# Kernel tuning notes

Hardware: AMD Instinct MI355X
Metric: run time of the kernel (lower is better)

The kernel has to match this reference:

```python
import jax, jax.numpy as jnp
import numpy as np

DIM = 2048
NUM_EXPERTS = 4
EPS = 1e-6
SCALE = 3.0


def setup_inputs() -> dict:
    key = jax.random.key(0)
    k_x, k_w = jax.random.split(key)
    x = jax.random.normal(k_x, (4, 8192, DIM), dtype=jnp.float32)
    norm_weight = jnp.ones((DIM,), dtype=jnp.float32)
    router_weight = jax.random.normal(k_w, (NUM_EXPERTS, DIM), dtype=jnp.float32) * (1.0 / np.sqrt(DIM))
    return {"x": x, "norm_weight": norm_weight, "router_weight": router_weight}


def reference(x, norm_weight, router_weight):
    # RMSNorm over last dim
    rms = jnp.sqrt(jnp.mean(x * x, axis=-1, keepdims=True) + EPS)
    xn = x / rms * norm_weight
    # tiny router projection: [b, s, d] @ [e, d]^T -> [b, s, e]
    logits = jnp.einsum('bsd,ed->bse', xn, router_weight) * SCALE
    return jnp.tanh(logits)
```

## Files before the change

### kernel.cpp

```cpp
#include <hip/hip_runtime.h>
#include <cmath>

constexpr int   DIM   = 2048;
constexpr int   NEXP  = 4;
constexpr float EPS   = 1e-6f;
constexpr float SCALE = 3.0f;

__global__ __launch_bounds__(256, 2)
void altup_router_kernel(const float* __restrict__ x,
                         const float* __restrict__ nw,
                         const float* __restrict__ rw,
                         float* __restrict__ out,
                         int nrows)
{
    const int lane          = threadIdx.x & 63;
    const int wid_in_blk    = threadIdx.x >> 6;
    const int waves_per_blk = blockDim.x >> 6;
    const int nwaves        = gridDim.x * waves_per_blk;
    const int wave          = blockIdx.x * waves_per_blk + wid_in_blk;

    const int base = lane * 4;

    float4 w[NEXP][8];
#pragma unroll
    for (int e = 0; e < NEXP; ++e) {
#pragma unroll
        for (int k = 0; k < 8; ++k) {
            const int d = k * 256 + base;
            const float4 r = *reinterpret_cast<const float4*>(rw + e * DIM + d);
            const float4 n = *reinterpret_cast<const float4*>(nw + d);
            w[e][k] = make_float4(r.x * n.x, r.y * n.y, r.z * n.z, r.w * n.w);
        }
    }

    for (int row = wave; row < nrows; row += nwaves) {
        const float* xr = x + (size_t)row * DIM;

        float acc[5] = {0.f, 0.f, 0.f, 0.f, 0.f};
#pragma unroll
        for (int k = 0; k < 8; ++k) {
            const float4 xv = *reinterpret_cast<const float4*>(xr + k * 256 + base);

            acc[0] = fmaf(xv.x, xv.x, acc[0]);
            acc[0] = fmaf(xv.y, xv.y, acc[0]);
            acc[0] = fmaf(xv.z, xv.z, acc[0]);
            acc[0] = fmaf(xv.w, xv.w, acc[0]);
#pragma unroll
            for (int e = 0; e < NEXP; ++e) {
                acc[1 + e] = fmaf(xv.x, w[e][k].x, acc[1 + e]);
                acc[1 + e] = fmaf(xv.y, w[e][k].y, acc[1 + e]);
                acc[1 + e] = fmaf(xv.z, w[e][k].z, acc[1 + e]);
                acc[1 + e] = fmaf(xv.w, w[e][k].w, acc[1 + e]);
            }
        }

#pragma unroll
        for (int m = 32; m >= 1; m >>= 1) {
#pragma unroll
            for (int i = 0; i < 5; ++i)
                acc[i] += __shfl_xor(acc[i], m, 64);
        }

        if (lane == 0) {
            const float inv_rms = rsqrtf(acc[0] * (1.0f / DIM) + EPS);
            float4 o;
            o.x = tanhf(acc[1] * inv_rms * SCALE);
            o.y = tanhf(acc[2] * inv_rms * SCALE);
            o.z = tanhf(acc[3] * inv_rms * SCALE);
            o.w = tanhf(acc[4] * inv_rms * SCALE);
            reinterpret_cast<float4*>(out)[row] = o;
        }
    }
}

extern "C" void kernel_launch(void* const* d_in, const int* in_sizes, int n_in,
                              void* d_out, int out_size, void* d_ws, size_t ws_size,
                              hipStream_t stream)
{
    const float* x   = (const float*)d_in[0];
    const float* nw  = (const float*)d_in[1];
    const float* rw  = (const float*)d_in[2];
    float*       out = (float*)d_out;

    const int nrows = in_sizes[0] / DIM;

    int waves_needed  = (nrows + 7) / 8;
    int blocks        = (waves_needed + 3) / 4;
    if (blocks > 1024) blocks = 1024;
    if (blocks < 1)    blocks = 1;

    hipLaunchKernelGGL(altup_router_kernel, dim3(blocks), dim3(256), 0, stream,
                       x, nw, rw, out, nrows);
}
```

Measured before the change: 49.30 us.

## Stage router weights in LDS and process two rows per wave

```diff
diff --git a/kernel.cpp b/kernel.cpp
--- a/kernel.cpp
+++ b/kernel.cpp
@@ -6,69 +6,97 @@
 constexpr float EPS   = 1e-6f;
 constexpr float SCALE = 3.0f;
 
-__global__ __launch_bounds__(256, 2)
+__global__ __launch_bounds__(256, 4)
 void altup_router_kernel(const float* __restrict__ x,
                          const float* __restrict__ nw,
                          const float* __restrict__ rw,
                          float* __restrict__ out,
                          int nrows)
 {
-    const int lane          = threadIdx.x & 63;
-    const int wid_in_blk    = threadIdx.x >> 6;
-    const int waves_per_blk = blockDim.x >> 6;
-    const int nwaves        = gridDim.x * waves_per_blk;
-    const int wave          = blockIdx.x * waves_per_blk + wid_in_blk;
+    __shared__ float wlds[NEXP * DIM];
 
-    const int base = lane * 4;
+    const int tid = threadIdx.x;
 
-    float4 w[NEXP][8];
-#pragma unroll
-    for (int e = 0; e < NEXP; ++e) {
+    for (int i = tid * 4; i < NEXP * DIM; i += 256 * 4) {
+        const int d = i & (DIM - 1);
+        const float4 r = *reinterpret_cast<const float4*>(rw + i);
+        const float4 n = *reinterpret_cast<const float4*>(nw + d);
+        *reinterpret_cast<float4*>(wlds + i) =
+            make_float4(r.x * n.x, r.y * n.y, r.z * n.z, r.w * n.w);
+    }
+    __syncthreads();
+
+    const int lane   = tid & 63;
+    const int wid    = tid >> 6;
+    const int nwaves = gridDim.x * (blockDim.x >> 6);
+    const int wave   = blockIdx.x * (blockDim.x >> 6) + wid;
+    const int base   = lane * 4;
+
+    const int npairs = (nrows + 1) >> 1;
+
+    for (int pr = wave; pr < npairs; pr += nwaves) {
+        const int row  = pr * 2;
+        const bool two = (row + 1) < nrows;
+
+        const float* xr0 = x + (size_t)row * DIM;
+        const float* xr1 = xr0 + (two ? DIM : 0);
+
+        float acc[10] = {0.f};
+
 #pragma unroll
         for (int k = 0; k < 8; ++k) {
             const int d = k * 256 + base;
-            const float4 r = *reinterpret_cast<const float4*>(rw + e * DIM + d);
-            const float4 n = *reinterpret_cast<const float4*>(nw + d);
-            w[e][k] = make_float4(r.x * n.x, r.y * n.y, r.z * n.z, r.w * n.w);
-        }
-    }
+            const float4 a = *reinterpret_cast<const float4*>(xr0 + d);
+            const float4 b = *reinterpret_cast<const float4*>(xr1 + d);
 
-    for (int row = wave; row < nrows; row += nwaves) {
-        const float* xr = x + (size_t)row * DIM;
+            acc[0] = fmaf(a.x, a.x, acc[0]);
+            acc[0] = fmaf(a.y, a.y, acc[0]);
+            acc[0] = fmaf(a.z, a.z, acc[0]);
+            acc[0] = fmaf(a.w, a.w, acc[0]);
+            acc[5] = fmaf(b.x, b.x, acc[5]);
+            acc[5] = fmaf(b.y, b.y, acc[5]);
+            acc[5] = fmaf(b.z, b.z, acc[5]);
+            acc[5] = fmaf(b.w, b.w, acc[5]);
 
-        float acc[5] = {0.f, 0.f, 0.f, 0.f, 0.f};
-#pragma unroll
-        for (int k = 0; k < 8; ++k) {
-            const float4 xv = *reinterpret_cast<const float4*>(xr + k * 256 + base);
-
-            acc[0] = fmaf(xv.x, xv.x, acc[0]);
-            acc[0] = fmaf(xv.y, xv.y, acc[0]);
-            acc[0] = fmaf(xv.z, xv.z, acc[0]);
-            acc[0] = fmaf(xv.w, xv.w, acc[0]);
 #pragma unroll
             for (int e = 0; e < NEXP; ++e) {
-                acc[1 + e] = fmaf(xv.x, w[e][k].x, acc[1 + e]);
-                acc[1 + e] = fmaf(xv.y, w[e][k].y, acc[1 + e]);
-                acc[1 + e] = fmaf(xv.z, w[e][k].z, acc[1 + e]);
-                acc[1 + e] = fmaf(xv.w, w[e][k].w, acc[1 + e]);
+                const float4 w = *reinterpret_cast<const float4*>(wlds + e * DIM + d);
+                acc[1 + e] = fmaf(a.x, w.x, acc[1 + e]);
+                acc[1 + e] = fmaf(a.y, w.y, acc[1 + e]);
+                acc[1 + e] = fmaf(a.z, w.z, acc[1 + e]);
+                acc[1 + e] = fmaf(a.w, w.w, acc[1 + e]);
+                acc[6 + e] = fmaf(b.x, w.x, acc[6 + e]);
+                acc[6 + e] = fmaf(b.y, w.y, acc[6 + e]);
+                acc[6 + e] = fmaf(b.z, w.z, acc[6 + e]);
+                acc[6 + e] = fmaf(b.w, w.w, acc[6 + e]);
             }
         }
 
 #pragma unroll
         for (int m = 32; m >= 1; m >>= 1) {
 #pragma unroll
-            for (int i = 0; i < 5; ++i)
+            for (int i = 0; i < 10; ++i)
                 acc[i] += __shfl_xor(acc[i], m, 64);
         }
 
         if (lane == 0) {
-            const float inv_rms = rsqrtf(acc[0] * (1.0f / DIM) + EPS);
-            float4 o;
-            o.x = tanhf(acc[1] * inv_rms * SCALE);
-            o.y = tanhf(acc[2] * inv_rms * SCALE);
-            o.z = tanhf(acc[3] * inv_rms * SCALE);
-            o.w = tanhf(acc[4] * inv_rms * SCALE);
-            reinterpret_cast<float4*>(out)[row] = o;
+            const float ir0 = rsqrtf(acc[0] * (1.0f / DIM) + EPS);
+            float4 o0;
+            o0.x = tanhf(acc[1] * ir0 * SCALE);
+            o0.y = tanhf(acc[2] * ir0 * SCALE);
+            o0.z = tanhf(acc[3] * ir0 * SCALE);
+            o0.w = tanhf(acc[4] * ir0 * SCALE);
+            reinterpret_cast<float4*>(out)[row] = o0;
+
+            if (two) {
+                const float ir1 = rsqrtf(acc[5] * (1.0f / DIM) + EPS);
+                float4 o1;
+                o1.x = tanhf(acc[6] * ir1 * SCALE);
+                o1.y = tanhf(acc[7] * ir1 * SCALE);
+                o1.z = tanhf(acc[8] * ir1 * SCALE);
+                o1.w = tanhf(acc[9] * ir1 * SCALE);
+                reinterpret_cast<float4*>(out)[row + 1] = o1;
+            }
         }
     }
 }
@@ -82,12 +110,13 @@
     const float* rw  = (const float*)d_in[2];
     float*       out = (float*)d_out;
 
-    const int nrows = in_sizes[0] / DIM;
+    const int nrows  = in_sizes[0] / DIM;
+    const int npairs = (nrows + 1) >> 1;
 
-    int waves_needed  = (nrows + 7) / 8;
-    int blocks        = (waves_needed + 3) / 4;
-    if (blocks > 1024) blocks = 1024;
-    if (blocks < 1)    blocks = 1;
+    int blocks = 512;
+    const int max_blocks = (npairs + 3) / 4;
+    if (blocks > max_blocks) blocks = max_blocks;
+    if (blocks < 1) blocks = 1;
 
     hipLaunchKernelGGL(altup_router_kernel, dim3(blocks), dim3(256), 0, stream,
                        x, nw, rw, out, nrows);
```

Result: slower. 117.1 us (+137.5%).

## Double-buffer row loads with contiguous per-wave chunks and nontemporal loads

Applied to the files above, without the earlier changes.

```diff
diff --git a/kernel.cpp b/kernel.cpp
--- a/kernel.cpp
+++ b/kernel.cpp
@@ -6,70 +6,91 @@
 constexpr float EPS   = 1e-6f;
 constexpr float SCALE = 3.0f;
 
+typedef float f32x4 __attribute__((ext_vector_type(4)));
+
 __global__ __launch_bounds__(256, 2)
 void altup_router_kernel(const float* __restrict__ x,
                          const float* __restrict__ nw,
                          const float* __restrict__ rw,
                          float* __restrict__ out,
-                         int nrows)
+                         int nrows, int chunk)
 {
-    const int lane          = threadIdx.x & 63;
-    const int wid_in_blk    = threadIdx.x >> 6;
-    const int waves_per_blk = blockDim.x >> 6;
-    const int nwaves        = gridDim.x * waves_per_blk;
-    const int wave          = blockIdx.x * waves_per_blk + wid_in_blk;
-
+    const int tid  = threadIdx.x;
+    const int lane = tid & 63;
+    const int wid  = tid >> 6;
+    const int wave = blockIdx.x * (blockDim.x >> 6) + wid;
     const int base = lane * 4;
 
-    float4 w[NEXP][8];
+    f32x4 w[NEXP][8];
 #pragma unroll
     for (int e = 0; e < NEXP; ++e) {
 #pragma unroll
         for (int k = 0; k < 8; ++k) {
             const int d = k * 256 + base;
-            const float4 r = *reinterpret_cast<const float4*>(rw + e * DIM + d);
-            const float4 n = *reinterpret_cast<const float4*>(nw + d);
-            w[e][k] = make_float4(r.x * n.x, r.y * n.y, r.z * n.z, r.w * n.w);
+            const f32x4 r = *reinterpret_cast<const f32x4*>(rw + e * DIM + d);
+            const f32x4 n = *reinterpret_cast<const f32x4*>(nw + d);
+            w[e][k] = r * n;
         }
     }
 
-    for (int row = wave; row < nrows; row += nwaves) {
+    int r    = wave * chunk;
+    int rend = r + chunk;
+    if (rend > nrows) rend = nrows;
+    if (r >= rend) return;
+
+    f32x4 bufA[8], bufB[8];
+
+    auto LOAD = [&](f32x4 (&buf)[8], int row) {
         const float* xr = x + (size_t)row * DIM;
+#pragma unroll
+        for (int k = 0; k < 8; ++k)
+            buf[k] = __builtin_nontemporal_load(
+                         reinterpret_cast<const f32x4*>(xr + k * 256 + base));
+    };
 
+    auto PROC = [&](const f32x4 (&buf)[8], int row) {
         float acc[5] = {0.f, 0.f, 0.f, 0.f, 0.f};
 #pragma unroll
         for (int k = 0; k < 8; ++k) {
-            const float4 xv = *reinterpret_cast<const float4*>(xr + k * 256 + base);
-
-            acc[0] = fmaf(xv.x, xv.x, acc[0]);
-            acc[0] = fmaf(xv.y, xv.y, acc[0]);
-            acc[0] = fmaf(xv.z, xv.z, acc[0]);
-            acc[0] = fmaf(xv.w, xv.w, acc[0]);
+            const f32x4 a = buf[k];
+#pragma unroll
+            for (int j = 0; j < 4; ++j)
+                acc[0] = fmaf(a[j], a[j], acc[0]);
 #pragma unroll
             for (int e = 0; e < NEXP; ++e) {
-                acc[1 + e] = fmaf(xv.x, w[e][k].x, acc[1 + e]);
-                acc[1 + e] = fmaf(xv.y, w[e][k].y, acc[1 + e]);
-                acc[1 + e] = fmaf(xv.z, w[e][k].z, acc[1 + e]);
-                acc[1 + e] = fmaf(xv.w, w[e][k].w, acc[1 + e]);
+                const f32x4 we = w[e][k];
+#pragma unroll
+                for (int j = 0; j < 4; ++j)
+                    acc[1 + e] = fmaf(a[j], we[j], acc[1 + e]);
             }
         }
-
 #pragma unroll
         for (int m = 32; m >= 1; m >>= 1) {
 #pragma unroll
             for (int i = 0; i < 5; ++i)
                 acc[i] += __shfl_xor(acc[i], m, 64);
         }
+        if (lane == 0) {
+            const float ir = rsqrtf(acc[0] * (1.0f / DIM) + EPS);
+            f32x4 o;
+            o.x = tanhf(acc[1] * ir * SCALE);
+            o.y = tanhf(acc[2] * ir * SCALE);
+            o.z = tanhf(acc[3] * ir * SCALE);
+            o.w = tanhf(acc[4] * ir * SCALE);
+            *reinterpret_cast<f32x4*>(out + (size_t)row * 4) = o;
+        }
+    };
 
-        if (lane == 0) {
-            const float inv_rms = rsqrtf(acc[0] * (1.0f / DIM) + EPS);
-            float4 o;
-            o.x = tanhf(acc[1] * inv_rms * SCALE);
-            o.y = tanhf(acc[2] * inv_rms * SCALE);
-            o.z = tanhf(acc[3] * inv_rms * SCALE);
-            o.w = tanhf(acc[4] * inv_rms * SCALE);
-            reinterpret_cast<float4*>(out)[row] = o;
-        }
+    LOAD(bufA, r);
+    for (;;) {
+        if (r + 1 < rend) LOAD(bufB, r + 1);
+        PROC(bufA, r);
+        ++r;
+        if (r >= rend) break;
+        if (r + 1 < rend) LOAD(bufA, r + 1);
+        PROC(bufB, r);
+        ++r;
+        if (r >= rend) break;
     }
 }
 
@@ -84,11 +105,16 @@
 
     const int nrows = in_sizes[0] / DIM;
 
-    int waves_needed  = (nrows + 7) / 8;
-    int blocks        = (waves_needed + 3) / 4;
-    if (blocks > 1024) blocks = 1024;
-    if (blocks < 1)    blocks = 1;
+    int blocks = 512;
+    int nwaves = blocks * 4;
+    if (nwaves > nrows) {
+        nwaves = nrows;
+        blocks = (nwaves + 3) / 4;
+        if (blocks < 1) blocks = 1;
+        nwaves = blocks * 4;
+    }
+    const int chunk = (nrows + nwaves - 1) / nwaves;
 
     hipLaunchKernelGGL(altup_router_kernel, dim3(blocks), dim3(256), 0, stream,
-                       x, nw, rw, out, nrows);
+                       x, nw, rw, out, nrows, chunk);
 }
```

Result: slower. 52.29 us (+6.1%).
